# Performance work log

Hardware: AMD Instinct MI355X
Metric: run time of the kernel (lower is better)

## Reference

```python
import jax, jax.numpy as jnp
import numpy as np

B, S, D = 2, 2048, 1024
H, DK = 16, 64          # n_heads, head dim
HI, DI = 4, 64          # indexer heads, indexer dim
TOP_K = 512
ROPE_BASE = 10000.0


def _rope(x):
    # x: [B, S, H, DK]  (torchtune-style interleaved rotary)
    half = DK // 2
    theta = 1.0 / (ROPE_BASE ** (jnp.arange(0, DK, 2, dtype=jnp.float32) / DK))  # [half]
    ang = jnp.arange(S, dtype=jnp.float32)[:, None] * theta[None, :]             # [S, half]
    cos = jnp.cos(ang)[None, :, None, :].astype(x.dtype)                          # [1,S,1,half]
    sin = jnp.sin(ang)[None, :, None, :].astype(x.dtype)
    xs = x.reshape(x.shape[:-1] + (half, 2))
    x1, x2 = xs[..., 0], xs[..., 1]
    out = jnp.stack([x1 * cos - x2 * sin, x2 * cos + x1 * sin], axis=-1)
    return out.reshape(x.shape)


def setup_inputs() -> dict:
    key = jax.random.key(0)
    ks = jax.random.split(key, 6)
    std = 0.02
    return {
        "x": jax.random.normal(ks[0], (B, S, D), dtype=jnp.float32),
        "Wqkv": jax.random.normal(ks[1], (D, 3 * D), dtype=jnp.float32) * std,
        "Wo": jax.random.normal(ks[2], (D, D), dtype=jnp.float32) * std,
        "Wq_idx": jax.random.normal(ks[3], (D, HI * DI), dtype=jnp.float32) * std,
        "Wk_idx": jax.random.normal(ks[4], (D, DI), dtype=jnp.float32) * std,
        "Ww_idx": jax.random.normal(ks[5], (D, HI), dtype=jnp.float32) * std,
    }


def reference(x, Wqkv, Wo, Wq_idx, Wk_idx, Ww_idx):
    # ---- main QKV + RoPE ----
    qkv = (x @ Wqkv).reshape(B, S, 3, H, DK)
    q, k, v = qkv[:, :, 0], qkv[:, :, 1], qkv[:, :, 2]  # [B,S,H,DK]
    q = _rope(q)
    k = _rope(k)
    Q = q.transpose(0, 2, 1, 3)  # [B,H,S,DK]
    K = k.transpose(0, 2, 1, 3)
    V = v.transpose(0, 2, 1, 3)

    # ---- lightning indexer: I[b,t,s] = sum_h w[b,t,h] * relu(q_i . k_i) ----
    qi = (x @ Wq_idx).reshape(B, S, HI, DI)
    ki = x @ Wk_idx                              # [B,S,DI]
    w = x @ Ww_idx                               # [B,S,HI]
    dots = jnp.einsum("bthd,bsd->bths", qi, ki)  # [B,S,HI,S]
    index_scores = jnp.einsum("bths,bth->bts", jax.nn.relu(dots), w)

    # ---- top-k token selection (causal penalty of -1e9, as in original) ----
    causal = jnp.triu(jnp.ones((S, S), dtype=bool), k=1)
    masked_scores = jnp.where(causal[None], -1e9, index_scores)
    _, top_idx = jax.lax.top_k(masked_scores, TOP_K)  # [B,S,TOP_K]
    b_idx = jnp.arange(B)[:, None, None]
    t_idx = jnp.arange(S)[None, :, None]
    sel_mask = jnp.zeros((B, S, S), dtype=bool).at[b_idx, t_idx, top_idx].set(True)

    # ---- masked SDPA over full S^2 (additive mask, replicating original) ----
    add_mask = jnp.where(sel_mask[:, None], 0.0, -jnp.inf).astype(Q.dtype)  # [B,1,S,S]
    logits = jnp.einsum("bhtd,bhsd->bhts", Q, K) / jnp.sqrt(jnp.float32(DK)).astype(Q.dtype)
    probs = jax.nn.softmax(logits + add_mask, axis=-1)
    attn = jnp.einsum("bhts,bhsd->bhtd", probs, V)       # [B,H,S,DK]
    attn = attn.transpose(0, 2, 1, 3).reshape(B, S, D)
    return attn @ Wo
```

## Files before the change

kernel.cpp:

```cpp
#include <hip/hip_runtime.h>
#include <hip/hip_fp16.h>
#include <hip/hip_bf16.h>
#include <math.h>

#define BB 2
#define SS 2048
#define HH 16
#define TOPK 512
#define ROWS (BB*SS)
#define KDIM 1024
#define KP 3072
#define NSTR 384

using bf16x8 = __attribute__((ext_vector_type(8))) short;
using f32x4  = __attribute__((ext_vector_type(4))) float;
typedef _Float16 f16x8 __attribute__((ext_vector_type(8)));
typedef unsigned int u32;

__device__ __forceinline__ void gload16(const void* g, void* l) {
  __builtin_amdgcn_global_load_lds(
      (const __attribute__((address_space(1))) u32*)g,
      (__attribute__((address_space(3))) u32*)l, 16, 0, 0);
}

__device__ __forceinline__ void split_bf16(float f, short& hi, short& lo) {
  __hip_bfloat16 h = __float2bfloat16(f);
  float fh = __bfloat162float(h);
  __hip_bfloat16 l = __float2bfloat16(f - fh);
  hi = *reinterpret_cast<short*>(&h);
  lo = *reinterpret_cast<short*>(&l);
}

__device__ __forceinline__ unsigned fkey(float f) {
  unsigned u = __float_as_uint(f);
  if ((u << 1) == 0u) u = 0u;
  return (u & 0x80000000u) ? ~u : (u | 0x80000000u);
}

__global__ void rope_tab_k(float* __restrict__ ct, float* __restrict__ st) {
  int idx = blockIdx.x * blockDim.x + threadIdx.x;
  if (idx >= SS * 32) return;
  int s = idx >> 5, j = idx & 31;
  float theta = 1.0f / powf(10000.0f, (float)(2 * j) / 64.0f);
  float ang = (float)s * theta;
  float sv, cv;
  sincosf(ang, &sv, &cv);
  ct[idx] = cv;
  st[idx] = sv;
}

__global__ __launch_bounds__(256) void pack_a_k(
    const float* __restrict__ X, short* __restrict__ A, int total4)
{
  int idx = blockIdx.x * 256 + threadIdx.x;
  if (idx >= total4) return;
  float4 v = ((const float4*)X)[idx];
  float a4[4] = {v.x, v.y, v.z, v.w};
  short o[12];
#pragma unroll
  for (int j = 0; j < 4; ++j) {
    short hs, ls; split_bf16(a4[j], hs, ls);
    o[3*j] = hs; o[3*j+1] = hs; o[3*j+2] = ls;
  }
  short* op = A + (size_t)idx * 12;
  *(short4*)(op)     = *(short4*)&o[0];
  *(short4*)(op + 4) = *(short4*)&o[4];
  *(short4*)(op + 8) = *(short4*)&o[8];
}

__global__ __launch_bounds__(256) void pack_bt_k(
    const float* __restrict__ W, short* __restrict__ BT, int Nw)
{
  __shared__ float tile[32][33];
  int kb = blockIdx.y * 32, nb = blockIdx.x * 32;
  int tx = threadIdx.x & 31, ty = threadIdx.x >> 5;
  for (int yy = ty; yy < 32; yy += 8) {
    float v = 0.f;
    if (nb + tx < Nw) v = W[(size_t)(kb + yy) * Nw + nb + tx];
    tile[yy][tx] = v;
  }
  __syncthreads();
  for (int yy = ty; yy < 32; yy += 8) {
    int n = nb + yy;
    if (n >= Nw) continue;
    int k = kb + tx;
    float f = tile[tx][yy];
    short hs, ls; split_bf16(f, hs, ls);
    short* orow = BT + (size_t)n * KP + 3 * k;
    orow[0] = hs; orow[1] = ls; orow[2] = hs;
  }
}

__global__ __launch_bounds__(256) void pack_wcat_k(
    const float* __restrict__ Wq, const float* __restrict__ Wk,
    const float* __restrict__ Ww, float* __restrict__ Wcat)
{
  int idx = blockIdx.x * 256 + threadIdx.x;
  if (idx >= 1024 * NSTR) return;
  int k = idx / NSTR, n = idx - k * NSTR;
  float v = 0.f;
  if (n < 256)      v = Wq[(size_t)k * 256 + n];
  else if (n < 320) v = Wk[(size_t)k * 64 + (n - 256)];
  else if (n < 324) v = Ww[(size_t)k * 4 + (n - 320)];
  Wcat[idx] = v;
}

__global__ __launch_bounds__(256) void gemm_bf16h(
    const short* __restrict__ A, const short* __restrict__ BT,
    __half* __restrict__ C, int M, int N, int Kp, int kLen)
{
  __shared__ short As[128 * 64];
  __shared__ short Bs[128 * 64];
  const int tid = threadIdx.x;
  const int lane = tid & 63;
  const int wv = tid >> 6;
  const int m0 = blockIdx.y * 128, n0 = blockIdx.x * 128;
  const int z = blockIdx.z;
  const int kBeg = z * kLen;
  __half* Cp = C + (size_t)z * M * N;
  const int wr = (wv >> 1) * 64, wc = (wv & 1) * 64;
  f32x4 acc[4][4];
#pragma unroll
  for (int i = 0; i < 4; ++i)
#pragma unroll
    for (int j = 0; j < 4; ++j)
#pragma unroll
      for (int r = 0; r < 4; ++r) acc[i][j][r] = 0.0f;

  const int rsel = lane & 15;
  const int lrow = lane >> 3;
  const int lcol = (lane & 7) * 8;
  for (int k0 = kBeg; k0 < kBeg + kLen; k0 += 64) {
#pragma unroll
    for (int q = 0; q < 4; ++q) {
      int c = wv * 4 + q;
      int row = c * 8 + lrow;
      gload16(A  + (size_t)(m0 + row) * Kp + k0 + lcol, &As[c * 512]);
      gload16(BT + (size_t)(n0 + row) * Kp + k0 + lcol, &Bs[c * 512]);
    }
    __syncthreads();
#pragma unroll
    for (int kk = 0; kk < 2; ++kk) {
      bf16x8 af[4], bfr[4];
      int kof = kk * 32 + (lane >> 4) * 8;
#pragma unroll
      for (int i = 0; i < 4; ++i) {
        af[i]  = *(const bf16x8*)&As[(wr + i * 16 + rsel) * 64 + kof];
        bfr[i] = *(const bf16x8*)&Bs[(wc + i * 16 + rsel) * 64 + kof];
      }
#pragma unroll
      for (int i = 0; i < 4; ++i)
#pragma unroll
        for (int j = 0; j < 4; ++j)
          acc[i][j] = __builtin_amdgcn_mfma_f32_16x16x32_bf16(af[i], bfr[j], acc[i][j], 0, 0, 0);
    }
    __syncthreads();
  }
  const int er = m0 + wr + (lane >> 4) * 4;
  const int ec = n0 + wc + rsel;
#pragma unroll
  for (int i = 0; i < 4; ++i)
#pragma unroll
    for (int j = 0; j < 4; ++j)
#pragma unroll
      for (int r = 0; r < 4; ++r)
        Cp[(size_t)(er + i * 16 + r) * N + ec + j * 16] = __float2half_rn(acc[i][j][r]);
}

__global__ __launch_bounds__(128) void gemm_idx_k(
    const float* __restrict__ A, const float* __restrict__ Bw, float* __restrict__ C)
{
  __shared__ float As[16][36];
  __shared__ float Bs[16][68];
  int n0 = blockIdx.x * 64, m0 = blockIdx.y * 32;
  int tid = threadIdx.x;
  int tr = tid >> 4;
  int tc = tid & 15;
  float acc[4][4];
#pragma unroll
  for (int i = 0; i < 4; ++i)
#pragma unroll
    for (int j = 0; j < 4; ++j) acc[i][j] = 0.f;

  for (int k0 = 0; k0 < 1024; k0 += 16) {
    {
      int lin = tid * 4;
      int row = lin >> 4, kk = lin & 15;
      float4 av = *(const float4*)(A + (size_t)(m0 + row) * 1024 + k0 + kk);
      As[kk + 0][row] = av.x; As[kk + 1][row] = av.y;
      As[kk + 2][row] = av.z; As[kk + 3][row] = av.w;
      int lin2 = tid * 8;
      int bk = lin2 >> 6, bc = lin2 & 63;
      const float* bp = Bw + (size_t)(k0 + bk) * NSTR + n0 + bc;
      *(float4*)&Bs[bk][bc]     = *(const float4*)(bp);
      *(float4*)&Bs[bk][bc + 4] = *(const float4*)(bp + 4);
    }
    __syncthreads();
#pragma unroll
    for (int k = 0; k < 16; ++k) {
      float a[4], b[4];
      *(float4*)&a[0] = *(const float4*)&As[k][tr * 4];
      *(float4*)&b[0] = *(const float4*)&Bs[k][tc * 4];
#pragma unroll
      for (int i = 0; i < 4; ++i)
#pragma unroll
        for (int j = 0; j < 4; ++j)
          acc[i][j] = fmaf(a[i], b[j], acc[i][j]);
    }
    __syncthreads();
  }
#pragma unroll
  for (int i = 0; i < 4; ++i)
    *(float4*)(C + (size_t)(m0 + tr * 4 + i) * NSTR + n0 + tc * 4) = *(float4*)&acc[i][0];
}

__global__ __launch_bounds__(256) void qkv_post_k(
    const __half* __restrict__ P, const float* __restrict__ ct, const float* __restrict__ st,
    __half* __restrict__ Qh, __half* __restrict__ Kh, __half* __restrict__ Vh)
{
  int idx = blockIdx.x * 256 + threadIdx.x;
  if (idx >= ROWS * 384) return;
  int m = idx / 384;
  int g = idx - m * 384;
  int col0 = g * 8;
  const __half* c0 = P + (size_t)m * 3072 + col0;
  const __half* c1 = c0 + (size_t)ROWS * 3072;
  float4 u = *(const float4*)c0;
  float4 v = *(const float4*)c1;
  const __half2* hu = (const __half2*)&u;
  const __half2* hv = (const __half2*)&v;
  float a[8];
#pragma unroll
  for (int c = 0; c < 4; ++c) {
    float2 x = __half22float2(hu[c]);
    float2 y = __half22float2(hv[c]);
    a[2*c]   = x.x + y.x;
    a[2*c+1] = x.y + y.y;
  }
  int sec = col0 >> 10;
  int cin = col0 & 1023;
  size_t orow = (size_t)m * 1024 + cin;
  if (sec == 2) {
    __half2 hh[4];
#pragma unroll
    for (int c = 0; c < 4; ++c) hh[c] = __floats2half2_rn(a[2*c], a[2*c+1]);
    *(float4*)(Vh + orow) = *(float4*)hh;
  } else {
    int t = m & (SS - 1);
    int jb = (cin & 63) >> 1;
    float o[8];
#pragma unroll
    for (int c = 0; c < 4; ++c) {
      float cv = ct[t * 32 + jb + c], sv = st[t * 32 + jb + c];
      float x1 = a[2*c], x2 = a[2*c+1];
      o[2*c]   = x1 * cv - x2 * sv;
      o[2*c+1] = x2 * cv + x1 * sv;
    }
    if (sec == 0) {
#pragma unroll
      for (int c = 0; c < 8; ++c) o[c] *= 0.125f;
    }
    __half2 hh[4];
#pragma unroll
    for (int c = 0; c < 4; ++c) hh[c] = __floats2half2_rn(o[2*c], o[2*c+1]);
    __half* dst = (sec == 0) ? Qh : Kh;
    *(float4*)(dst + orow) = *(float4*)hh;
  }
}

__global__ __launch_bounds__(256) void vt_k(
    const __half* __restrict__ Vh, __half* __restrict__ VhT)
{
  int st = blockIdx.x, bh = blockIdx.y;
  int b = bh >> 4, h = bh & 15;
  int s0 = st * 64;
  __shared__ __half tile[64][65];
  int tid = threadIdx.x;
#pragma unroll
  for (int rnd = 0; rnd < 2; ++rnd) {
    int row = (tid >> 3) + rnd * 32;
    int c8 = (tid & 7) * 8;
    *(float4*)&tile[row][c8] =
        *(const float4*)(Vh + ((size_t)b * SS + s0 + row) * 1024 + h * 64 + c8);
  }
  __syncthreads();
#pragma unroll
  for (int rnd = 0; rnd < 2; ++rnd) {
    int d = (tid >> 3) + rnd * 32;
    int s8 = (tid & 7) * 8;
    __half tmp[8];
#pragma unroll
    for (int j = 0; j < 8; ++j) tmp[j] = tile[s8 + j][d];
    *(float4*)(VhT + ((size_t)bh * 64 + d) * 2048 + s0 + s8) = *(float4*)tmp;
  }
}

__global__ __launch_bounds__(256) void idx_topk_k(
    const float* __restrict__ Ccat, u32* __restrict__ msk)
{
  int t = blockIdx.x, b = blockIdx.y;
  int tid = threadIdx.x;
  int lane = tid & 63;
  int wv = tid >> 6;
  if (t < TOPK) {
    if (tid < 64)
      msk[((size_t)b * SS + t) * 64 + tid] = (tid < 16) ? 0xFFFFFFFFu : 0u;
    return;
  }
  __shared__ u32 uk[SS];
  __shared__ u32 hist[256];
  __shared__ u32 w[64];
  __shared__ u32 s_bsel, s_above;

  if (tid < 64) w[tid] = 0u;

  const float4* qrow = (const float4*)(Ccat + ((size_t)b * SS + t) * NSTR);
  const float* wrow = Ccat + ((size_t)b * SS + t) * NSTR + 320;
  float w0 = wrow[0], w1 = wrow[1], w2 = wrow[2], w3 = wrow[3];

#pragma unroll 1
  for (int s0 = 0; s0 <= t; s0 += 256) {
    int s = s0 + tid;
    if (s <= t) {
      const float4* kp = (const float4*)(Ccat + ((size_t)b * SS + s) * NSTR + 256);
      float a0 = 0.f, a1 = 0.f, a2 = 0.f, a3 = 0.f;
#pragma unroll
      for (int d4 = 0; d4 < 16; ++d4) {
        float4 kv = kp[d4];
        float4 q0 = qrow[d4];
        float4 q1 = qrow[16 + d4];
        float4 q2 = qrow[32 + d4];
        float4 q3 = qrow[48 + d4];
        a0 += q0.x * kv.x + q0.y * kv.y + q0.z * kv.z + q0.w * kv.w;
        a1 += q1.x * kv.x + q1.y * kv.y + q1.z * kv.z + q1.w * kv.w;
        a2 += q2.x * kv.x + q2.y * kv.y + q2.z * kv.z + q2.w * kv.w;
        a3 += q3.x * kv.x + q3.y * kv.y + q3.z * kv.z + q3.w * kv.w;
      }
      float v = fmaxf(a0, 0.f) * w0 + fmaxf(a1, 0.f) * w1 +
                fmaxf(a2, 0.f) * w2 + fmaxf(a3, 0.f) * w3;
      uk[s] = fkey(v);
    }
  }

  unsigned krem = TOPK;
  unsigned prefix = 0;
#pragma unroll 1
  for (int p = 0; p < 4; ++p) {
    int shift = 24 - 8 * p;
    u32 maskAbove = (p == 0) ? 0u : (0xFFFFFFFFu << (shift + 8));
    hist[tid] = 0u;
    __syncthreads();
#pragma unroll 1
    for (int s0 = 0; s0 <= t; s0 += 256) {
      int s = s0 + tid;
      if (s <= t) {
        u32 key = uk[s];
        if ((key & maskAbove) == prefix)
          atomicAdd(&hist[(key >> shift) & 255], 1u);
      }
    }
    __syncthreads();
    if (wv == 0) {
      uint4 hv = *(uint4*)&hist[lane * 4];
      u32 lsum = hv.x + hv.y + hv.z + hv.w;
      u32 x = lsum;
#pragma unroll
      for (int off = 1; off < 64; off <<= 1) {
        u32 y = __shfl_down(x, off);
        x += (lane + off < 64) ? y : 0u;
      }
      u32 esuf = x - lsum;
      u32 S3 = esuf + hv.w;
      u32 S2 = S3 + hv.z;
      u32 S1 = S2 + hv.y;
      u32 S0 = S1 + hv.x;
      if (S0 >= krem && S1 < krem)  { s_bsel = lane * 4 + 0; s_above = S1; }
      if (S1 >= krem && S2 < krem)  { s_bsel = lane * 4 + 1; s_above = S2; }
      if (S2 >= krem && S3 < krem)  { s_bsel = lane * 4 + 2; s_above = S3; }
      if (S3 >= krem && esuf < krem){ s_bsel = lane * 4 + 3; s_above = esuf; }
    }
    __syncthreads();
    prefix |= (s_bsel << shift);
    krem -= s_above;
  }

  u32 Tkey = prefix;
  unsigned kfin = krem;

#pragma unroll 1
  for (int s0 = 0; s0 <= t; s0 += 256) {
    int s = s0 + tid;
    bool pred = (s <= t) && (uk[s] > Tkey);
    unsigned long long mba = __ballot(pred);
    int wbase = (s0 + wv * 64) >> 5;
    if (lane == 0 && (u32)mba) atomicOr(&w[wbase], (u32)mba);
    if (lane == 32 && (u32)(mba >> 32)) atomicOr(&w[wbase + 1], (u32)(mba >> 32));
  }
  if (wv == 0) {
    unsigned taken = 0;
#pragma unroll 1
    for (int s0 = 0; s0 <= t && taken < kfin; s0 += 64) {
      int s = s0 + lane;
      bool pred = (s <= t) && (uk[s] == Tkey);
      unsigned long long mba = __ballot(pred);
      unsigned pre = (unsigned)__popcll(mba & ((1ull << lane) - 1ull));
      if (pred && (taken + pre) < kfin)
        atomicOr(&w[s >> 5], 1u << (s & 31));
      taken += (unsigned)__popcll(mba);
    }
  }
  __syncthreads();
  if (tid < 64) msk[((size_t)b * SS + t) * 64 + tid] = w[tid];
}

__global__ __launch_bounds__(256) void attn_dense_k(
    const __half* __restrict__ Qh, const __half* __restrict__ Kh,
    const __half* __restrict__ VhT, const u32* __restrict__ msk,
    short* __restrict__ Aattn)
{
  int bid = blockIdx.x;
  int xcd = bid & 7, loc = bid >> 3;
  int bh = xcd * 4 + (loc >> 5);
  int qt = loc & 31;
  int b = bh >> 4, h = bh & 15;
  int t0 = qt * 64;

  const int tid = threadIdx.x;
  const int lane = tid & 63;
  const int wv = tid >> 6;
  const int l15 = lane & 15;
  const int g = lane >> 4;

  __shared__ short lds[12800];
  short* Ks = lds;
  short* Vt = lds + 4096;
  short* Ps = lds + 8192 + wv * 1088;
  u32* mlds = (u32*)(lds + 12544);

  const size_t brow = (size_t)b * SS;

  f16x8 qf0, qf1;
  {
    const __half* qp = Qh + (brow + t0 + wv * 16 + l15) * 1024 + h * 64 + g * 8;
    qf0 = *(const f16x8*)(qp);
    qf1 = *(const f16x8*)(qp + 32);
  }

  f32x4 accO[4];
#pragma unroll
  for (int n2 = 0; n2 < 4; ++n2)
#pragma unroll
    for (int r = 0; r < 4; ++r) accO[n2][r] = 0.f;
  float mRun[4] = {-1e30f, -1e30f, -1e30f, -1e30f};
  float sRun[4] = {0.f, 0.f, 0.f, 0.f};

  const int srow = lane >> 3;
  const int scp  = (lane & 7) ^ srow;

#pragma unroll 1
  for (int kt = 0; kt < 32; ++kt) {
    int kt0 = kt * 64;
#pragma unroll
    for (int q = 0; q < 2; ++q) {
      int j = wv * 2 + q;
      gload16(Kh + (brow + kt0 + j * 8 + srow) * 1024 + h * 64 + scp * 8, Ks + j * 512);
      gload16(VhT + ((size_t)(bh * 64 + j * 8 + srow)) * 2048 + kt0 + scp * 8, Vt + j * 512);
    }
    if (tid < 128)
      mlds[tid] = msk[(brow + t0 + (tid >> 1)) * 64 + kt * 2 + (tid & 1)];
    __syncthreads();

    f32x4 s4[4];
#pragma unroll
    for (int ns = 0; ns < 4; ++ns) {
#pragma unroll
      for (int r = 0; r < 4; ++r) s4[ns][r] = 0.f;
      int rowk = ns * 16 + l15;
      int cp0 = g ^ (rowk & 7);
      int cp1 = (4 + g) ^ (rowk & 7);
      f16x8 kf0 = *(const f16x8*)&Ks[rowk * 64 + cp0 * 8];
      f16x8 kf1 = *(const f16x8*)&Ks[rowk * 64 + cp1 * 8];
      s4[ns] = __builtin_amdgcn_mfma_f32_16x16x32_f16(qf0, kf0, s4[ns], 0, 0, 0);
      s4[ns] = __builtin_amdgcn_mfma_f32_16x16x32_f16(qf1, kf1, s4[ns], 0, 0, 0);
    }

#pragma unroll
    for (int r = 0; r < 4; ++r) {
      int qb2 = (wv * 16 + g * 4 + r) * 2;
      u32 w0 = mlds[qb2];
      u32 w1 = mlds[qb2 + 1];
      float le[4];
#pragma unroll
      for (int ns = 0; ns < 4; ++ns) {
        u32 w = (ns < 2) ? w0 : w1;
        int bit = (ns & 1) * 16 + l15;
        float l = s4[ns][r];
        le[ns] = ((w >> bit) & 1u) ? l : -1e30f;
      }
      float cm = fmaxf(fmaxf(le[0], le[1]), fmaxf(le[2], le[3]));
      cm = fmaxf(cm, __shfl_xor(cm, 1));
      cm = fmaxf(cm, __shfl_xor(cm, 2));
      cm = fmaxf(cm, __shfl_xor(cm, 4));
      cm = fmaxf(cm, __shfl_xor(cm, 8));
      float mn = fmaxf(mRun[r], cm);
      float fac = __expf(mRun[r] - mn);
      mRun[r] = mn;
      float sum = 0.f;
#pragma unroll
      for (int ns = 0; ns < 4; ++ns) {
        float ee = __expf(le[ns] - mn);
        ee = (le[ns] < -1e29f) ? 0.f : ee;
        sum += ee;
        Ps[(g * 4 + r) * 68 + ns * 16 + l15] =
            (short)__half_as_ushort(__float2half_rn(ee));
      }
      sum += __shfl_xor(sum, 1);
      sum += __shfl_xor(sum, 2);
      sum += __shfl_xor(sum, 4);
      sum += __shfl_xor(sum, 8);
      sRun[r] = sRun[r] * fac + sum;
#pragma unroll
      for (int n2 = 0; n2 < 4; ++n2) accO[n2][r] *= fac;
    }

    f16x8 pa0, pa1;
    {
      const short* pp = &Ps[l15 * 68 + g * 8];
      float2 lo0 = *(const float2*)(pp);
      float2 hi0 = *(const float2*)(pp + 4);
      float2 lo1 = *(const float2*)(pp + 32);
      float2 hi1 = *(const float2*)(pp + 36);
      float4 c0 = make_float4(lo0.x, lo0.y, hi0.x, hi0.y);
      float4 c1 = make_float4(lo1.x, lo1.y, hi1.x, hi1.y);
      pa0 = *(const f16x8*)&c0;
      pa1 = *(const f16x8*)&c1;
    }
#pragma unroll
    for (int n2 = 0; n2 < 4; ++n2) {
      int rowd = n2 * 16 + l15;
      int cp0 = g ^ (rowd & 7);
      int cp1 = (4 + g) ^ (rowd & 7);
      f16x8 vf0 = *(const f16x8*)&Vt[rowd * 64 + cp0 * 8];
      f16x8 vf1 = *(const f16x8*)&Vt[rowd * 64 + cp1 * 8];
      accO[n2] = __builtin_amdgcn_mfma_f32_16x16x32_f16(pa0, vf0, accO[n2], 0, 0, 0);
      accO[n2] = __builtin_amdgcn_mfma_f32_16x16x32_f16(pa1, vf1, accO[n2], 0, 0, 0);
    }
    __syncthreads();
  }

#pragma unroll
  for (int r = 0; r < 4; ++r) {
    float inv = 1.0f / sRun[r];
    size_t grow = brow + t0 + wv * 16 + g * 4 + r;
    short* arow = Aattn + grow * 3072;
#pragma unroll
    for (int n2 = 0; n2 < 4; ++n2) {
      int col = h * 64 + n2 * 16 + l15;
      float v = accO[n2][r] * inv;
      short hs, ls; split_bf16(v, hs, ls);
      short* ap = arow + 3 * col;
      ap[0] = hs; ap[1] = hs; ap[2] = ls;
    }
  }
}

__global__ __launch_bounds__(256) void redout_k(
    const __half* __restrict__ O, float* __restrict__ out)
{
  int idx = blockIdx.x * 256 + threadIdx.x;
  if (idx >= ROWS * 1024 / 8) return;
  const size_t PS = (size_t)ROWS * 1024;
  float4 u0 = *((const float4*)O + idx);
  float4 u1 = *((const float4*)(O + PS) + idx);
  float4 u2 = *((const float4*)(O + 2 * PS) + idx);
  const __half2* h0 = (const __half2*)&u0;
  const __half2* h1 = (const __half2*)&u1;
  const __half2* h2 = (const __half2*)&u2;
  float o[8];
#pragma unroll
  for (int c = 0; c < 4; ++c) {
    float2 a = __half22float2(h0[c]);
    float2 b = __half22float2(h1[c]);
    float2 d = __half22float2(h2[c]);
    o[2*c]   = a.x + b.x + d.x;
    o[2*c+1] = a.y + b.y + d.y;
  }
  float* op = out + (size_t)idx * 8;
  *(float4*)(op)     = make_float4(o[0], o[1], o[2], o[3]);
  *(float4*)(op + 4) = make_float4(o[4], o[5], o[6], o[7]);
}

extern "C" void kernel_launch(void* const* d_in, const int* in_sizes, int n_in,
                              void* d_out, int out_size, void* d_ws, size_t ws_size,
                              hipStream_t stream) {
  const float* x    = (const float*)d_in[0];
  const float* Wqkv = (const float*)d_in[1];
  const float* Wo   = (const float*)d_in[2];
  const float* Wq   = (const float*)d_in[3];
  const float* Wk   = (const float*)d_in[4];
  const float* Ww   = (const float*)d_in[5];
  float* out = (float*)d_out;

  float* fws = (float*)d_ws;
  size_t o = 0;
  __half* Qh    = (__half*)(fws + o);  o += (size_t)ROWS * 512;
  __half* Kh    = (__half*)(fws + o);  o += (size_t)ROWS * 512;
  __half* Vh    = (__half*)(fws + o);  o += (size_t)ROWS * 512;
  float*  ct    = fws + o;             o += (size_t)SS * 32;
  float*  st    = fws + o;             o += (size_t)SS * 32;
  float*  Ccat  = fws + o;             o += (size_t)ROWS * NSTR;
  short*  BTwo  = (short*)(fws + o);   o += (size_t)1024 * KP / 2;
  short*  BTq   = (short*)(fws + o);   o += (size_t)3072 * KP / 2;
  short*  Ax    = (short*)(fws + o);
  float*  Wcat  = fws + o + (size_t)ROWS * 1024;
                      o += (size_t)ROWS * KP / 2;
  __half* Ph    = (__half*)(fws + o);
  short*  Aattn = (short*)(fws + o);
  __half* VhT   = (__half*)(fws + o + (size_t)8 * 1024 * 1024);
  u32*    msk   = (u32*)(fws + o + (size_t)10500 * 1024);
  o += (size_t)ROWS * 3072;
  __half* Oparts = (__half*)Qh;

  rope_tab_k<<<dim3((SS * 32 + 255) / 256), dim3(256), 0, stream>>>(ct, st);

  pack_a_k<<<dim3(ROWS * KDIM / 4 / 256), dim3(256), 0, stream>>>(x, Ax, ROWS * KDIM / 4);
  pack_bt_k<<<dim3(3072 / 32, 32), dim3(256), 0, stream>>>(Wqkv, BTq, 3072);
  pack_bt_k<<<dim3(1024 / 32, 32), dim3(256), 0, stream>>>(Wo, BTwo, 1024);

  gemm_bf16h<<<dim3(3072 / 128, ROWS / 128, 2), dim3(256), 0, stream>>>(
      Ax, BTq, Ph, ROWS, 3072, KP, KP / 2);
  qkv_post_k<<<dim3((ROWS * 384 + 255) / 256), dim3(256), 0, stream>>>(Ph, ct, st, Qh, Kh, Vh);
  vt_k<<<dim3(SS / 64, BB * HH), dim3(256), 0, stream>>>(Vh, VhT);

  pack_wcat_k<<<dim3((1024 * NSTR + 255) / 256), dim3(256), 0, stream>>>(Wq, Wk, Ww, Wcat);
  gemm_idx_k<<<dim3(NSTR / 64, ROWS / 32), dim3(128), 0, stream>>>(x, Wcat, Ccat);

  idx_topk_k<<<dim3(SS, BB), dim3(256), 0, stream>>>(Ccat, msk);
  attn_dense_k<<<dim3(1024), dim3(256), 0, stream>>>(Qh, Kh, VhT, msk, Aattn);

  gemm_bf16h<<<dim3(1024 / 128, ROWS / 128, 3), dim3(256), 0, stream>>>(
      Aattn, BTwo, Oparts, ROWS, 1024, KP, KP / 3);
  redout_k<<<dim3(ROWS * 1024 / 8 / 256), dim3(256), 0, stream>>>(Oparts, out);
}
```

Before: 537.6 us.

## Pair low and high query rows per block in indexer top-k to balance causal work

Each block of the indexer top-k kernel now handles two query rows, t and S-1-t, so every block does a similar amount of causal work and the grid is halved. The key vectors are loaded once and shared by both rows' dot products, and the query rows are staged in shared memory. The radix-select pass then runs for each row in turn. In exchange, shared memory doubles (two key arrays), per-thread register use rises, and the selection phases now run one after the other inside a block.

```diff
diff --git a/kernel.cpp b/kernel.cpp
--- a/kernel.cpp
+++ b/kernel.cpp
@@ -298,119 +298,152 @@
 __global__ __launch_bounds__(256) void idx_topk_k(
     const float* __restrict__ Ccat, u32* __restrict__ msk)
 {
-  int t = blockIdx.x, b = blockIdx.y;
+  int bx = blockIdx.x, b = blockIdx.y;
   int tid = threadIdx.x;
   int lane = tid & 63;
   int wv = tid >> 6;
-  if (t < TOPK) {
-    if (tid < 64)
-      msk[((size_t)b * SS + t) * 64 + tid] = (tid < 16) ? 0xFFFFFFFFu : 0u;
-    return;
-  }
-  __shared__ u32 uk[SS];
+  const int tLo = bx;
+  const int tHi = SS - 1 - bx;
+  const bool hasLo = (tLo >= TOPK);
+
+  __shared__ u32 uk0[SS];
+  __shared__ u32 uk1[SS];
+  __shared__ float4 qsLo[64];
+  __shared__ float4 qsHi[64];
   __shared__ u32 hist[256];
   __shared__ u32 w[64];
   __shared__ u32 s_bsel, s_above;
 
-  if (tid < 64) w[tid] = 0u;
-
-  const float4* qrow = (const float4*)(Ccat + ((size_t)b * SS + t) * NSTR);
-  const float* wrow = Ccat + ((size_t)b * SS + t) * NSTR + 320;
-  float w0 = wrow[0], w1 = wrow[1], w2 = wrow[2], w3 = wrow[3];
+  if (!hasLo && tid < 64)
+    msk[((size_t)b * SS + tLo) * 64 + tid] = (tid < 16) ? 0xFFFFFFFFu : 0u;
+
+  const float4* qLo = (const float4*)(Ccat + ((size_t)b * SS + tLo) * NSTR);
+  const float4* qHi = (const float4*)(Ccat + ((size_t)b * SS + tHi) * NSTR);
+  if (tid < 64) qsLo[tid] = qLo[tid];
+  if (tid >= 64 && tid < 128) qsHi[tid - 64] = qHi[tid - 64];
+  const float* wLo = Ccat + ((size_t)b * SS + tLo) * NSTR + 320;
+  const float* wHi = Ccat + ((size_t)b * SS + tHi) * NSTR + 320;
+  float wl0 = wLo[0], wl1 = wLo[1], wl2 = wLo[2], wl3 = wLo[3];
+  float wh0 = wHi[0], wh1 = wHi[1], wh2 = wHi[2], wh3 = wHi[3];
+  __syncthreads();
 
 #pragma unroll 1
-  for (int s0 = 0; s0 <= t; s0 += 256) {
+  for (int s0 = 0; s0 <= tHi; s0 += 256) {
     int s = s0 + tid;
-    if (s <= t) {
+    if (s <= tHi) {
       const float4* kp = (const float4*)(Ccat + ((size_t)b * SS + s) * NSTR + 256);
-      float a0 = 0.f, a1 = 0.f, a2 = 0.f, a3 = 0.f;
-#pragma unroll
+      const bool vLo = hasLo && (s <= tLo);
+      float a10 = 0.f, a11 = 0.f, a12 = 0.f, a13 = 0.f;
+      float a00 = 0.f, a01 = 0.f, a02 = 0.f, a03 = 0.f;
+#pragma unroll 4
       for (int d4 = 0; d4 < 16; ++d4) {
         float4 kv = kp[d4];
-        float4 q0 = qrow[d4];
-        float4 q1 = qrow[16 + d4];
-        float4 q2 = qrow[32 + d4];
-        float4 q3 = qrow[48 + d4];
-        a0 += q0.x * kv.x + q0.y * kv.y + q0.z * kv.z + q0.w * kv.w;
-        a1 += q1.x * kv.x + q1.y * kv.y + q1.z * kv.z + q1.w * kv.w;
-        a2 += q2.x * kv.x + q2.y * kv.y + q2.z * kv.z + q2.w * kv.w;
-        a3 += q3.x * kv.x + q3.y * kv.y + q3.z * kv.z + q3.w * kv.w;
+        float4 q0 = qsHi[d4];
+        float4 q1 = qsHi[16 + d4];
+        float4 q2 = qsHi[32 + d4];
+        float4 q3 = qsHi[48 + d4];
+        a10 += q0.x * kv.x + q0.y * kv.y + q0.z * kv.z + q0.w * kv.w;
+        a11 += q1.x * kv.x + q1.y * kv.y + q1.z * kv.z + q1.w * kv.w;
+        a12 += q2.x * kv.x + q2.y * kv.y + q2.z * kv.z + q2.w * kv.w;
+        a13 += q3.x * kv.x + q3.y * kv.y + q3.z * kv.z + q3.w * kv.w;
+        if (vLo) {
+          float4 p0 = qsLo[d4];
+          float4 p1 = qsLo[16 + d4];
+          float4 p2 = qsLo[32 + d4];
+          float4 p3 = qsLo[48 + d4];
+          a00 += p0.x * kv.x + p0.y * kv.y + p0.z * kv.z + p0.w * kv.w;
+          a01 += p1.x * kv.x + p1.y * kv.y + p1.z * kv.z + p1.w * kv.w;
+          a02 += p2.x * kv.x + p2.y * kv.y + p2.z * kv.z + p2.w * kv.w;
+          a03 += p3.x * kv.x + p3.y * kv.y + p3.z * kv.z + p3.w * kv.w;
+        }
       }
-      float v = fmaxf(a0, 0.f) * w0 + fmaxf(a1, 0.f) * w1 +
-                fmaxf(a2, 0.f) * w2 + fmaxf(a3, 0.f) * w3;
-      uk[s] = fkey(v);
-    }
-  }
-
-  unsigned krem = TOPK;
-  unsigned prefix = 0;
+      uk1[s] = fkey(fmaxf(a10, 0.f) * wh0 + fmaxf(a11, 0.f) * wh1 +
+                    fmaxf(a12, 0.f) * wh2 + fmaxf(a13, 0.f) * wh3);
+      if (vLo)
+        uk0[s] = fkey(fmaxf(a00, 0.f) * wl0 + fmaxf(a01, 0.f) * wl1 +
+                      fmaxf(a02, 0.f) * wl2 + fmaxf(a03, 0.f) * wl3);
+    }
+  }
+  __syncthreads();
+
 #pragma unroll 1
-  for (int p = 0; p < 4; ++p) {
-    int shift = 24 - 8 * p;
-    u32 maskAbove = (p == 0) ? 0u : (0xFFFFFFFFu << (shift + 8));
-    hist[tid] = 0u;
-    __syncthreads();
+  for (int sel2 = 0; sel2 < 2; ++sel2) {
+    if (sel2 == 0 && !hasLo) continue;
+    u32* ukp = sel2 ? uk1 : uk0;
+    const int t = sel2 ? tHi : tLo;
+    if (tid < 64) w[tid] = 0u;
+
+    unsigned krem = TOPK;
+    unsigned prefix = 0;
+#pragma unroll 1
+    for (int p = 0; p < 4; ++p) {
+      int shift = 24 - 8 * p;
+      u32 maskAbove = (p == 0) ? 0u : (0xFFFFFFFFu << (shift + 8));
+      hist[tid] = 0u;
+      __syncthreads();
+#pragma unroll 1
+      for (int s0 = 0; s0 <= t; s0 += 256) {
+        int s = s0 + tid;
+        if (s <= t) {
+          u32 key = ukp[s];
+          if ((key & maskAbove) == prefix)
+            atomicAdd(&hist[(key >> shift) & 255], 1u);
+        }
+      }
+      __syncthreads();
+      if (wv == 0) {
+        uint4 hv = *(uint4*)&hist[lane * 4];
+        u32 lsum = hv.x + hv.y + hv.z + hv.w;
+        u32 x = lsum;
+#pragma unroll
+        for (int off = 1; off < 64; off <<= 1) {
+          u32 y = __shfl_down(x, off);
+          x += (lane + off < 64) ? y : 0u;
+        }
+        u32 esuf = x - lsum;
+        u32 S3 = esuf + hv.w;
+        u32 S2 = S3 + hv.z;
+        u32 S1 = S2 + hv.y;
+        u32 S0 = S1 + hv.x;
+        if (S0 >= krem && S1 < krem)  { s_bsel = lane * 4 + 0; s_above = S1; }
+        if (S1 >= krem && S2 < krem)  { s_bsel = lane * 4 + 1; s_above = S2; }
+        if (S2 >= krem && S3 < krem)  { s_bsel = lane * 4 + 2; s_above = S3; }
+        if (S3 >= krem && esuf < krem){ s_bsel = lane * 4 + 3; s_above = esuf; }
+      }
+      __syncthreads();
+      prefix |= (s_bsel << shift);
+      krem -= s_above;
+    }
+
+    u32 Tkey = prefix;
+    unsigned kfin = krem;
+
 #pragma unroll 1
     for (int s0 = 0; s0 <= t; s0 += 256) {
       int s = s0 + tid;
-      if (s <= t) {
-        u32 key = uk[s];
-        if ((key & maskAbove) == prefix)
-          atomicAdd(&hist[(key >> shift) & 255], 1u);
+      bool pred = (s <= t) && (ukp[s] > Tkey);
+      unsigned long long mba = __ballot(pred);
+      int wbase = (s0 + wv * 64) >> 5;
+      if (lane == 0 && (u32)mba) atomicOr(&w[wbase], (u32)mba);
+      if (lane == 32 && (u32)(mba >> 32)) atomicOr(&w[wbase + 1], (u32)(mba >> 32));
+    }
+    if (wv == 0) {
+      unsigned taken = 0;
+#pragma unroll 1
+      for (int s0 = 0; s0 <= t && taken < kfin; s0 += 64) {
+        int s = s0 + lane;
+        bool pred = (s <= t) && (ukp[s] == Tkey);
+        unsigned long long mba = __ballot(pred);
+        unsigned pre = (unsigned)__popcll(mba & ((1ull << lane) - 1ull));
+        if (pred && (taken + pre) < kfin)
+          atomicOr(&w[s >> 5], 1u << (s & 31));
+        taken += (unsigned)__popcll(mba);
       }
     }
     __syncthreads();
-    if (wv == 0) {
-      uint4 hv = *(uint4*)&hist[lane * 4];
-      u32 lsum = hv.x + hv.y + hv.z + hv.w;
-      u32 x = lsum;
-#pragma unroll
-      for (int off = 1; off < 64; off <<= 1) {
-        u32 y = __shfl_down(x, off);
-        x += (lane + off < 64) ? y : 0u;
-      }
-      u32 esuf = x - lsum;
-      u32 S3 = esuf + hv.w;
-      u32 S2 = S3 + hv.z;
-      u32 S1 = S2 + hv.y;
-      u32 S0 = S1 + hv.x;
-      if (S0 >= krem && S1 < krem)  { s_bsel = lane * 4 + 0; s_above = S1; }
-      if (S1 >= krem && S2 < krem)  { s_bsel = lane * 4 + 1; s_above = S2; }
-      if (S2 >= krem && S3 < krem)  { s_bsel = lane * 4 + 2; s_above = S3; }
-      if (S3 >= krem && esuf < krem){ s_bsel = lane * 4 + 3; s_above = esuf; }
-    }
-    __syncthreads();
-    prefix |= (s_bsel << shift);
-    krem -= s_above;
-  }
-
-  u32 Tkey = prefix;
-  unsigned kfin = krem;
-
-#pragma unroll 1
-  for (int s0 = 0; s0 <= t; s0 += 256) {
-    int s = s0 + tid;
-    bool pred = (s <= t) && (uk[s] > Tkey);
-    unsigned long long mba = __ballot(pred);
-    int wbase = (s0 + wv * 64) >> 5;
-    if (lane == 0 && (u32)mba) atomicOr(&w[wbase], (u32)mba);
-    if (lane == 32 && (u32)(mba >> 32)) atomicOr(&w[wbase + 1], (u32)(mba >> 32));
-  }
-  if (wv == 0) {
-    unsigned taken = 0;
-#pragma unroll 1
-    for (int s0 = 0; s0 <= t && taken < kfin; s0 += 64) {
-      int s = s0 + lane;
-      bool pred = (s <= t) && (uk[s] == Tkey);
-      unsigned long long mba = __ballot(pred);
-      unsigned pre = (unsigned)__popcll(mba & ((1ull << lane) - 1ull));
-      if (pred && (taken + pre) < kfin)
-        atomicOr(&w[s >> 5], 1u << (s & 31));
-      taken += (unsigned)__popcll(mba);
-    }
-  }
-  __syncthreads();
-  if (tid < 64) msk[((size_t)b * SS + t) * 64 + tid] = w[tid];
+    if (tid < 64) msk[((size_t)b * SS + t) * 64 + tid] = w[tid];
+    __syncthreads();
+  }
 }
 
 __global__ __launch_bounds__(256) void attn_dense_k(
@@ -635,7 +668,7 @@
   pack_wcat_k<<<dim3((1024 * NSTR + 255) / 256), dim3(256), 0, stream>>>(Wq, Wk, Ww, Wcat);
   gemm_idx_k<<<dim3(NSTR / 64, ROWS / 32), dim3(128), 0, stream>>>(x, Wcat, Ccat);
 
-  idx_topk_k<<<dim3(SS, BB), dim3(256), 0, stream>>>(Ccat, msk);
+  idx_topk_k<<<dim3(SS / 2, BB), dim3(256), 0, stream>>>(Ccat, msk);
   attn_dense_k<<<dim3(1024), dim3(256), 0, stream>>>(Qh, Kh, VhT, msk, Aattn);
 
   gemm_bf16h<<<dim3(1024 / 128, ROWS / 128, 3), dim3(256), 0, stream>>>(
```

New measurement: 629.8 us. 1.17x slower.
